# Performance work log

Measured on AMD Instinct MI355X. Metric: run time of the kernel, lower is better.

The kernel has to match this reference:

```python
import jax, jax.numpy as jnp
import numpy as np

# 4D conv dimension numbers: N=batch, C/I/O=channels, T,Z,Y,X = 4 spatial dims
DN = ('NCTZYX', 'OITZYX', 'NCTZYX')
PAD = [(1, 1)] * 4  # padding=1 on each of the 4 spatial dims


def setup_inputs() -> dict:
    key = jax.random.key(0)
    kx, kw = jax.random.split(key)
    B, Cin, Cout = 1, 16, 4
    T, D, H, Wd = 10, 32, 64, 64
    K = 3
    x = jax.random.normal(kx, (B, Cin, T, D, H, Wd), dtype=jnp.float32)
    # xavier_uniform over [Cout, Cin, 3,3,3,3]
    fan_in = Cin * K ** 4
    fan_out = Cout * K ** 4
    limit = float(np.sqrt(6.0 / (fan_in + fan_out)))
    W = jax.random.uniform(kw, (Cout, Cin, K, K, K, K), dtype=jnp.float32,
                           minval=-limit, maxval=limit)
    b = jnp.zeros((Cout,), dtype=jnp.float32)
    return {"x": x, "W": W, "b": b}


def reference(x, W, b):
    # True 4D convolution (stride 1, padding 1, 'same' output) + channel softmax
    y = jax.lax.conv_general_dilated(
        x, W,
        window_strides=(1, 1, 1, 1),
        padding=PAD,
        dimension_numbers=DN,
    )
    y = y + b[None, :, None, None, None, None]
    return jax.nn.softmax(y, axis=1)
```

## Files before the change

kernel.cpp:

```cpp
#include <hip/hip_runtime.h>
#include <hip/hip_bf16.h>

#define CIN  16
#define COUT 4
#define TT   10
#define ZZ   32
#define YY   64
#define XX   64

constexpr int SX_CI = TT * ZZ * YY * XX;
constexpr int SX_T  = ZZ * YY * XX;
constexpr int SX_Z  = YY * XX;
constexpr int WCO   = CIN * 81;

constexpr int XT_TB = ZZ * YY * XX * CIN * 2;
constexpr int XT_ZB = YY * XX * CIN * 2;
constexpr int XT_YB = XX * CIN * 2;
constexpr size_t XT_BYTES = (size_t)TT * XT_TB;
constexpr size_t BTAB     = XT_BYTES;
constexpr size_t ZOFF     = BTAB + 9 * 2048;
constexpr size_t WS_NEED  = ZOFF + 2048;

typedef short  short8 __attribute__((ext_vector_type(8)));
typedef float  f32x4  __attribute__((ext_vector_type(4)));

__device__ __forceinline__ unsigned short f2bf(float f) {
    union { __hip_bfloat16 h; unsigned short u; } c;
    c.h = __float2bfloat16(f);
    return c.u;
}
__device__ __forceinline__ unsigned int pk(float a, float b) {
    return (unsigned int)f2bf(a) | ((unsigned int)f2bf(b) << 16);
}

#define TXS 36
#define TYS (64 * TXS)
__global__ __launch_bounds__(256) void transpose_x(const float* __restrict__ x,
                                                   char* __restrict__ ws) {
    __shared__ char lds[16 * TYS];
    const int lane = threadIdx.x & 63;
    const int w    = threadIdx.x >> 6;
    const int yq = blockIdx.x, z = blockIdx.y, t = blockIdx.z;
    const int y0 = yq * 16;
    const int rl = w * 4 + (lane >> 4);
    const int x0 = (lane & 15) * 4;
    const size_t gbase = (size_t)t * SX_T + (size_t)z * SX_Z +
                         (size_t)(y0 + rl) * XX + x0;
#pragma unroll
    for (int cp = 0; cp < 8; ++cp) {
        const float4 f0 = *(const float4*)(x + (size_t)(2 * cp + 0) * SX_CI + gbase);
        const float4 f1 = *(const float4*)(x + (size_t)(2 * cp + 1) * SX_CI + gbase);
        char* p = lds + rl * TYS + x0 * TXS + cp * 4;
        *(unsigned int*)(p + 0 * TXS) = pk(f0.x, f1.x);
        *(unsigned int*)(p + 1 * TXS) = pk(f0.y, f1.y);
        *(unsigned int*)(p + 2 * TXS) = pk(f0.z, f1.z);
        *(unsigned int*)(p + 3 * TXS) = pk(f0.w, f1.w);
    }
    __syncthreads();
#pragma unroll
    for (int s = 0; s < 4; ++s) {
        const int r2 = w * 4 + s;
        char* rowp = ws + (((size_t)t * ZZ + z) * YY + (y0 + r2)) * 2048;
#pragma unroll
        for (int half = 0; half < 2; ++half) {
            const int c = half * 64 + lane;
            const uint4 d = *(const uint4*)(lds + r2 * TYS + (c >> 1) * TXS +
                                            (c & 1) * 16);
            *(uint4*)(rowp + c * 16) = d;
        }
    }
}

__global__ void prep_B(const float* __restrict__ W, char* __restrict__ ws) {
    const int g = blockIdx.x * 256 + threadIdx.x;
    if (g < 1152) {
        const int p = g >> 7, rem = g & 127, frag = rem >> 6, L = rem & 63;
        const int q = L >> 4, n = L & 15, co = n & 3, dx = n >> 2;
        const int dt = p / 3, dz = p % 3;
        unsigned int d[4];
#pragma unroll
        for (int j = 0; j < 4; ++j) {
            float v0 = 0.f, v1 = 0.f;
            if (dx < 3) {
                if (frag == 0) {
                    const int dy = q >> 1;
                    const int ci0 = (q & 1) * 8 + 2 * j;
                    v0 = W[(co * CIN + ci0) * 81 + dt * 27 + dz * 9 + dy * 3 + dx];
                    v1 = W[(co * CIN + ci0 + 1) * 81 + dt * 27 + dz * 9 + dy * 3 + dx];
                } else if (q < 2) {
                    const int ci0 = q * 8 + 2 * j;
                    v0 = W[(co * CIN + ci0) * 81 + dt * 27 + dz * 9 + 6 + dx];
                    v1 = W[(co * CIN + ci0 + 1) * 81 + dt * 27 + dz * 9 + 6 + dx];
                }
            }
            d[j] = pk(v0, v1);
        }
        *(uint4*)(ws + BTAB + (size_t)p * 2048 + frag * 1024 + (size_t)L * 16) =
            make_uint4(d[0], d[1], d[2], d[3]);
    } else if (g < 1280) {
        *(uint4*)(ws + ZOFF + (size_t)(g - 1152) * 16) = make_uint4(0, 0, 0, 0);
    }
}

#define GL16(SRC, DST) __builtin_amdgcn_global_load_lds( \
    (const __attribute__((address_space(1))) unsigned int*)(SRC), \
    (__attribute__((address_space(3))) unsigned int*)(DST), 16, 0, 0)

#define LROW 21
__global__ __launch_bounds__(256, 4) void conv_mfma(
        const char* __restrict__ ws,
        const float* __restrict__ bias,
        float* __restrict__ out) {
    __shared__ char smem[18 * 2048];
    const int lane = threadIdx.x;
    const int wid  = __builtin_amdgcn_readfirstlane(threadIdx.y);
    const int yq = blockIdx.x, z0 = blockIdx.y, t0 = blockIdx.z;
    const int y0 = yq * 16;
    const int m = lane & 15, q = lane >> 4, h = q & 1, dyA = q >> 1;
    const int e2 = 2 * m + h;
    const int wid4 = wid * 4;

    f32x4 acc[4][4];
#pragma unroll
    for (int r = 0; r < 4; ++r)
#pragma unroll
        for (int xt = 0; xt < 4; ++xt) acc[r][xt] = (f32x4){0.f, 0.f, 0.f, 0.f};

#define STAGE(P) { \
    const int dtS = (P) / 3, dzS = (P) % 3; \
    const int t_in = t0 + dtS - 1, z_in = z0 + dzS - 1; \
    const bool pv = ((unsigned)t_in < TT) && ((unsigned)z_in < ZZ); \
    const int pbase = pv ? (t_in * XT_TB + z_in * XT_ZB) : 0; \
    _Pragma("unroll") \
    for (int k = 0; k < 9; ++k) { \
        const int rw = (wid + 4 * k) >> 1; \
        const int hf = ((wid + 4 * k) & 1) * 1024; \
        const int y_in = y0 - 1 + rw; \
        const bool rv = pv && ((unsigned)y_in < YY); \
        const char* srcS = ws + (rv ? (size_t)(pbase + y_in * XT_YB) : ZOFF) \
                              + hf + lane * 16; \
        GL16(srcS, smem + rw * 2048 + hf + lane * 16); \
    } }

#define COMPUTE(P) { \
    const short8 BfA = *(const short8*)(ws + BTAB + (P) * 2048 + lane * 16); \
    const short8 BfB = *(const short8*)(ws + BTAB + (P) * 2048 + 1024 + lane * 16); \
    _Pragma("unroll") \
    for (int r = 0; r < 4; ++r) { \
        _Pragma("unroll") \
        for (int xt = 0; xt < 4; ++xt) { \
            const int sw = (32 * xt + e2) * 16; \
            const short8 fa = *(const short8*)(smem + (wid4 + r + dyA) * 2048 + sw); \
            const short8 fb = *(const short8*)(smem + (wid4 + r + 2) * 2048 + sw); \
            acc[r][xt] = __builtin_amdgcn_mfma_f32_16x16x32_bf16(fa, BfA, acc[r][xt], 0, 0, 0); \
            acc[r][xt] = __builtin_amdgcn_mfma_f32_16x16x32_bf16(fb, BfB, acc[r][xt], 0, 0, 0); \
        } } }

    STAGE(0) __syncthreads(); COMPUTE(0) __syncthreads();
    STAGE(1) __syncthreads(); COMPUTE(1) __syncthreads();
    STAGE(2) __syncthreads(); COMPUTE(2) __syncthreads();
    STAGE(3) __syncthreads(); COMPUTE(3) __syncthreads();
    STAGE(4) __syncthreads(); COMPUTE(4) __syncthreads();
    STAGE(5) __syncthreads(); COMPUTE(5) __syncthreads();
    STAGE(6) __syncthreads(); COMPUTE(6) __syncthreads();
    STAGE(7) __syncthreads(); COMPUTE(7) __syncthreads();
    STAGE(8) __syncthreads(); COMPUTE(8) __syncthreads();
#undef STAGE
#undef COMPUTE

    const float bi0 = bias[0], bi1 = bias[1], bi2 = bias[2], bi3 = bias[3];
    float* swave = (float*)smem + wid * (66 * LROW);
    if (lane < LROW) {
        swave[lane] = 0.f;
        swave[65 * LROW + lane] = 0.f;
    }
    const int colw = lane & 15;
    const int rowq = (lane >> 4) * 4 + 1;
#pragma unroll
    for (int r = 0; r < 4; ++r) {
#pragma unroll
        for (int xt = 0; xt < 4; ++xt)
#pragma unroll
            for (int reg = 0; reg < 4; ++reg)
                swave[(xt * 16 + rowq + reg) * LROW + colw] = acc[r][xt][reg];
        float lg0 = bi0, lg1 = bi1, lg2 = bi2, lg3 = bi3;
#pragma unroll
        for (int dx = 0; dx < 3; ++dx) {
            const float* sp = swave + (lane + dx) * LROW + dx * 4;
            lg0 += sp[0]; lg1 += sp[1]; lg2 += sp[2]; lg3 += sp[3];
        }
        const float mx = fmaxf(fmaxf(lg0, lg1), fmaxf(lg2, lg3));
        const float e0 = __expf(lg0 - mx);
        const float e1 = __expf(lg1 - mx);
        const float e2v = __expf(lg2 - mx);
        const float e3 = __expf(lg3 - mx);
        const float inv = 1.f / (e0 + e1 + e2v + e3);
        const int y = y0 + wid4 + r;
        float* op = out + (size_t)t0 * SX_T + (size_t)z0 * SX_Z + (size_t)y * XX + lane;
        op[0 * (size_t)SX_CI] = e0 * inv;
        op[1 * (size_t)SX_CI] = e1 * inv;
        op[2 * (size_t)SX_CI] = e2v * inv;
        op[3 * (size_t)SX_CI] = e3 * inv;
    }
}

__global__ __launch_bounds__(256, 4) void conv4d_softmax_vec(
        const float* __restrict__ x, const float* __restrict__ W,
        const float* __restrict__ b, float* __restrict__ out) {
    const int lane = threadIdx.x;
    const int xg = lane & 15, yl = lane >> 4;
    const int y = blockIdx.x * 16 + threadIdx.y * 4 + yl;
    const int z0 = blockIdx.y, t0 = blockIdx.z, x0 = xg * 4;
    float acc[COUT][4];
#pragma unroll
    for (int c = 0; c < COUT; ++c)
#pragma unroll
        for (int xi = 0; xi < 4; ++xi) acc[c][xi] = 0.f;
    for (int ci = 0; ci < CIN; ++ci) {
        const float* xc = x + (size_t)ci * SX_CI;
        const float* wc = W + ci * 81;
#pragma unroll
        for (int dt = 0; dt < 3; ++dt) {
            const int t_in = t0 + dt - 1;
            const int t_c = min(max(t_in, 0), TT - 1);
            const bool tv = (unsigned)t_in < TT;
#pragma unroll
            for (int dz = 0; dz < 3; ++dz) {
                const int z_in = z0 + dz - 1;
                const int z_c = min(max(z_in, 0), ZZ - 1);
                const bool tzvv = tv && ((unsigned)z_in < ZZ);
                const float* plane = xc + (size_t)t_c * SX_T + (size_t)z_c * SX_Z;
                const float* wb = wc + (dt * 3 + dz) * 9;
#pragma unroll
                for (int e = 0; e < 3; ++e) {
                    const int y_in = y + e - 1;
                    const int y_c = min(max(y_in, 0), YY - 1);
                    const bool v = tzvv && ((unsigned)y_in < YY);
                    float4 f = *(const float4*)(plane + y_c * XX + x0);
                    f.x = v ? f.x : 0.f; f.y = v ? f.y : 0.f;
                    f.z = v ? f.z : 0.f; f.w = v ? f.w : 0.f;
                    float hl = __shfl(f.w, (lane - 1) & 63, 64);
                    hl = (xg == 0) ? 0.f : hl;
                    float hr = __shfl(f.x, (lane + 1) & 63, 64);
                    hr = (xg == 15) ? 0.f : hr;
                    const float win[6] = {hl, f.x, f.y, f.z, f.w, hr};
#pragma unroll
                    for (int co = 0; co < COUT; ++co) {
                        const float* wp = wb + co * WCO + e * 3;
                        const float w0 = wp[0], w1 = wp[1], w2 = wp[2];
#pragma unroll
                        for (int xi = 0; xi < 4; ++xi) {
                            float a = acc[co][xi];
                            a = fmaf(win[xi], w0, a);
                            a = fmaf(win[xi + 1], w1, a);
                            a = fmaf(win[xi + 2], w2, a);
                            acc[co][xi] = a;
                        }
                    }
                }
            }
        }
    }
    const float b0 = b[0], b1 = b[1], b2 = b[2], b3 = b[3];
    float4 rr[COUT];
#pragma unroll
    for (int xi = 0; xi < 4; ++xi) {
        const float a0 = acc[0][xi] + b0, a1 = acc[1][xi] + b1;
        const float a2 = acc[2][xi] + b2, a3 = acc[3][xi] + b3;
        const float mm = fmaxf(fmaxf(a0, a1), fmaxf(a2, a3));
        const float e0 = __expf(a0 - mm), e1 = __expf(a1 - mm);
        const float e2 = __expf(a2 - mm), e3 = __expf(a3 - mm);
        const float inv = 1.f / (e0 + e1 + e2 + e3);
        ((float*)&rr[0])[xi] = e0 * inv; ((float*)&rr[1])[xi] = e1 * inv;
        ((float*)&rr[2])[xi] = e2 * inv; ((float*)&rr[3])[xi] = e3 * inv;
    }
    float* op = out + (size_t)t0 * SX_T + (size_t)z0 * SX_Z + (size_t)y * XX + x0;
#pragma unroll
    for (int co = 0; co < COUT; ++co)
        *(float4*)(op + (size_t)co * SX_CI) = rr[co];
}

extern "C" void kernel_launch(void* const* d_in, const int* in_sizes, int n_in,
                              void* d_out, int out_size, void* d_ws, size_t ws_size,
                              hipStream_t stream) {
    const float* x = (const float*)d_in[0];
    const float* W = (const float*)d_in[1];
    const float* b = (const float*)d_in[2];
    float* out = (float*)d_out;

    if (ws_size >= WS_NEED) {
        char* ws = (char*)d_ws;
        transpose_x<<<dim3(4, ZZ, TT), dim3(256), 0, stream>>>(x, ws);
        prep_B<<<dim3(5), dim3(256), 0, stream>>>(W, ws);
        conv_mfma<<<dim3(4, ZZ, TT), dim3(64, 4), 0, stream>>>(ws, b, out);
    } else {
        conv4d_softmax_vec<<<dim3(4, ZZ, TT), dim3(64, 4), 0, stream>>>(x, W, b, out);
    }
}
```

Before: 184.7 us.

## Double-buffer LDS staging and remap blocks to XCDs for z-locality

Splits the LDS tile into two buffers so the async global-to-LDS load for the next (dt,dz) plane overlaps the MFMA compute on the current one, which halves the barriers per stage. The grid is also flattened to 1D and remapped so that consecutive z-slices land on the same XCD, improving L2 reuse of the overlapping input planes. In exchange LDS use doubles to 72KB and the launch bound drops to 2 blocks per CU, lowering occupancy. The epilogue still reuses smem from offset 0, while the final compute reads buffer 0, and a barrier follows it.

```diff
diff --git a/kernel.cpp b/kernel.cpp
--- a/kernel.cpp
+++ b/kernel.cpp
@@ -107,14 +107,18 @@
     (__attribute__((address_space(3))) unsigned int*)(DST), 16, 0, 0)
 
 #define LROW 21
-__global__ __launch_bounds__(256, 4) void conv_mfma(
+__global__ __launch_bounds__(256, 2) void conv_mfma(
         const char* __restrict__ ws,
         const float* __restrict__ bias,
         float* __restrict__ out) {
-    __shared__ char smem[18 * 2048];
+    __shared__ char smem[2 * 18 * 2048];
     const int lane = threadIdx.x;
     const int wid  = __builtin_amdgcn_readfirstlane(threadIdx.y);
-    const int yq = blockIdx.x, z0 = blockIdx.y, t0 = blockIdx.z;
+    const int bid = blockIdx.x;
+    const int xcd = bid & 7, lid = bid >> 3;
+    const int z0 = 4 * xcd + (lid & 3);
+    const int yq = (lid >> 2) & 3;
+    const int t0 = lid >> 4;
     const int y0 = yq * 16;
     const int m = lane & 15, q = lane >> 4, h = q & 1, dyA = q >> 1;
     const int e2 = 2 * m + h;
@@ -126,7 +130,7 @@
 #pragma unroll
         for (int xt = 0; xt < 4; ++xt) acc[r][xt] = (f32x4){0.f, 0.f, 0.f, 0.f};
 
-#define STAGE(P) { \
+#define STAGE(P, BUF) { \
     const int dtS = (P) / 3, dzS = (P) % 3; \
     const int t_in = t0 + dtS - 1, z_in = z0 + dzS - 1; \
     const bool pv = ((unsigned)t_in < TT) && ((unsigned)z_in < ZZ); \
@@ -139,10 +143,11 @@
         const bool rv = pv && ((unsigned)y_in < YY); \
         const char* srcS = ws + (rv ? (size_t)(pbase + y_in * XT_YB) : ZOFF) \
                               + hf + lane * 16; \
-        GL16(srcS, smem + rw * 2048 + hf + lane * 16); \
+        GL16(srcS, smem + (BUF) * 36864 + rw * 2048 + hf + lane * 16); \
     } }
 
-#define COMPUTE(P) { \
+#define COMPUTE(P, BUF) { \
+    const char* bbC = smem + (BUF) * 36864; \
     const short8 BfA = *(const short8*)(ws + BTAB + (P) * 2048 + lane * 16); \
     const short8 BfB = *(const short8*)(ws + BTAB + (P) * 2048 + 1024 + lane * 16); \
     _Pragma("unroll") \
@@ -150,21 +155,22 @@
         _Pragma("unroll") \
         for (int xt = 0; xt < 4; ++xt) { \
             const int sw = (32 * xt + e2) * 16; \
-            const short8 fa = *(const short8*)(smem + (wid4 + r + dyA) * 2048 + sw); \
-            const short8 fb = *(const short8*)(smem + (wid4 + r + 2) * 2048 + sw); \
+            const short8 fa = *(const short8*)(bbC + (wid4 + r + dyA) * 2048 + sw); \
+            const short8 fb = *(const short8*)(bbC + (wid4 + r + 2) * 2048 + sw); \
             acc[r][xt] = __builtin_amdgcn_mfma_f32_16x16x32_bf16(fa, BfA, acc[r][xt], 0, 0, 0); \
             acc[r][xt] = __builtin_amdgcn_mfma_f32_16x16x32_bf16(fb, BfB, acc[r][xt], 0, 0, 0); \
         } } }
 
-    STAGE(0) __syncthreads(); COMPUTE(0) __syncthreads();
-    STAGE(1) __syncthreads(); COMPUTE(1) __syncthreads();
-    STAGE(2) __syncthreads(); COMPUTE(2) __syncthreads();
-    STAGE(3) __syncthreads(); COMPUTE(3) __syncthreads();
-    STAGE(4) __syncthreads(); COMPUTE(4) __syncthreads();
-    STAGE(5) __syncthreads(); COMPUTE(5) __syncthreads();
-    STAGE(6) __syncthreads(); COMPUTE(6) __syncthreads();
-    STAGE(7) __syncthreads(); COMPUTE(7) __syncthreads();
-    STAGE(8) __syncthreads(); COMPUTE(8) __syncthreads();
+    STAGE(0, 0) __syncthreads();
+    STAGE(1, 1) COMPUTE(0, 0) __syncthreads();
+    STAGE(2, 0) COMPUTE(1, 1) __syncthreads();
+    STAGE(3, 1) COMPUTE(2, 0) __syncthreads();
+    STAGE(4, 0) COMPUTE(3, 1) __syncthreads();
+    STAGE(5, 1) COMPUTE(4, 0) __syncthreads();
+    STAGE(6, 0) COMPUTE(5, 1) __syncthreads();
+    STAGE(7, 1) COMPUTE(6, 0) __syncthreads();
+    STAGE(8, 0) COMPUTE(7, 1) __syncthreads();
+    COMPUTE(8, 0) __syncthreads();
 #undef STAGE
 #undef COMPUTE
 
@@ -292,7 +298,7 @@
         char* ws = (char*)d_ws;
         transpose_x<<<dim3(4, ZZ, TT), dim3(256), 0, stream>>>(x, ws);
         prep_B<<<dim3(5), dim3(256), 0, stream>>>(W, ws);
-        conv_mfma<<<dim3(4, ZZ, TT), dim3(64, 4), 0, stream>>>(ws, b, out);
+        conv_mfma<<<dim3(1280), dim3(64, 4), 0, stream>>>(ws, b, out);
     } else {
         conv4d_softmax_vec<<<dim3(4, ZZ, TT), dim3(64, 4), 0, stream>>>(x, W, b, out);
     }
```

After: 171.6 us. 1.08x faster.
